# Optimization experiments

Hardware: AMD Instinct MI355X
Metric: run time of the kernel (lower is better)

The kernel has to match this reference:

```python
import jax, jax.numpy as jnp
import numpy as np


def setup_inputs() -> dict:
    key = jax.random.key(0)
    ks = jax.random.split(key, 6)
    N, C, T, V = 32, 64, 128, 25
    F = C * T * V  # 204800
    H = 256
    E = 4
    stdv0 = 1.0 / np.sqrt(F)
    stdv1 = 1.0 / np.sqrt(H)
    stdvA = 1.0 / np.sqrt(V)
    return {
        "x": jax.random.normal(ks[0], (N, C, T, V), dtype=jnp.float32),
        "W0": jax.random.uniform(ks[1], (F, H), jnp.float32, -stdv0, stdv0),
        "b0": jnp.zeros((H,), jnp.float32),
        "W1": jax.random.uniform(ks[2], (H, H), jnp.float32, -stdv1, stdv1),
        "b1": jnp.zeros((H,), jnp.float32),
        "W2": jax.random.uniform(ks[3], (H, E), jnp.float32, -stdv1, stdv1),
        "b2": jnp.zeros((E,), jnp.float32),
        "A": jax.random.uniform(ks[4], (E, T, V, V), jnp.float32, -stdvA, stdvA),
    }


def reference(x, W0, b0, W1, b1, W2, b2, A):
    N = x.shape[0]
    # Gating MLP (dropout treated as identity / eval mode)
    g = x.reshape(N, -1)                      # [N, C*T*V]
    h = jax.nn.elu(g @ W0 + b0)               # [N, 256]
    h = jax.nn.elu(h @ W1 + b1)               # [N, 256]
    logits = h @ W2 + b2                      # [N, 4]
    w = jax.nn.softmax(logits, axis=1)        # [N, 4]
    # Mixture of adjacency experts: AS[n,t,v,w] = sum_e w[n,e] * A[e,t,v,w]
    AS = jnp.einsum('ne,etvw->ntvw', w, A)    # [N, T, V, V]
    # Batched graph convolution
    out = jnp.einsum('nctv,ntvw->nctw', x, AS)
    return out
```

## Files before the change

### kernel.cpp

```cpp
#include <hip/hip_runtime.h>
#include <math.h>

#define Nn 32
#define Cc 64
#define Tt 128
#define Vv 25
#define Kk 204800
#define Hh 256
#define Ee 4
#define KC 256
#define NBLK_A 800

__device__ __forceinline__ float elu1(float v) { return v > 0.0f ? v : expm1f(v); }

__global__ __launch_bounds__(256) void kA(const float* __restrict__ x,
                                          const float* __restrict__ W0,
                                          float* __restrict__ partials) {
  __shared__ float xs[Nn][KC];
  const int tid = threadIdx.x;
  const int b = blockIdx.x;
  const int k0 = b * KC;

  #pragma unroll
  for (int j = tid; j < Nn * (KC / 4); j += 256) {
    int n = j >> 6;
    int c4 = j & 63;
    float4 v = *(const float4*)(x + (size_t)n * Kk + k0 + c4 * 4);
    *(float4*)&xs[n][c4 * 4] = v;
  }
  __syncthreads();

  const int hg = tid & 31;
  const int np = tid >> 5;
  const int h0 = hg * 8;
  const int n0 = np * 4;
  const float* W0p = W0 + (size_t)k0 * Hh + h0;

  float acc[4][8];
  #pragma unroll
  for (int i = 0; i < 4; ++i)
    #pragma unroll
    for (int c = 0; c < 8; ++c) acc[i][c] = 0.0f;

  for (int kk = 0; kk < KC; kk += 4) {
    float4 xv[4];
    #pragma unroll
    for (int i = 0; i < 4; ++i)
      xv[i] = *(const float4*)&xs[n0 + i][kk];
    #pragma unroll
    for (int u = 0; u < 4; ++u) {
      const float* wp = W0p + (size_t)(kk + u) * Hh;
      float4 wa = *(const float4*)(wp);
      float4 wb = *(const float4*)(wp + 4);
      #pragma unroll
      for (int i = 0; i < 4; ++i) {
        float xu = (u == 0) ? xv[i].x : (u == 1) ? xv[i].y : (u == 2) ? xv[i].z : xv[i].w;
        acc[i][0] = fmaf(xu, wa.x, acc[i][0]);
        acc[i][1] = fmaf(xu, wa.y, acc[i][1]);
        acc[i][2] = fmaf(xu, wa.z, acc[i][2]);
        acc[i][3] = fmaf(xu, wa.w, acc[i][3]);
        acc[i][4] = fmaf(xu, wb.x, acc[i][4]);
        acc[i][5] = fmaf(xu, wb.y, acc[i][5]);
        acc[i][6] = fmaf(xu, wb.z, acc[i][6]);
        acc[i][7] = fmaf(xu, wb.w, acc[i][7]);
      }
    }
  }
  #pragma unroll
  for (int i = 0; i < 4; ++i) {
    float* pp = partials + ((size_t)(b * Nn + n0 + i) << 8) + h0;
    *(float4*)(pp)     = make_float4(acc[i][0], acc[i][1], acc[i][2], acc[i][3]);
    *(float4*)(pp + 4) = make_float4(acc[i][4], acc[i][5], acc[i][6], acc[i][7]);
  }
}

__global__ __launch_bounds__(256) void kB1(const float* __restrict__ partials,
                                           const float* __restrict__ b0,
                                           float* __restrict__ hb) {
  const int n  = blockIdx.x >> 3;
  const int hc = blockIdx.x & 7;
  const int tid = threadIdx.x;
  const int hl = tid & 31;
  const int bsub = tid >> 5;
  const int h = hc * 32 + hl;
  float s = 0.0f;
  for (int j = 0; j < 100; ++j) {
    int b = bsub * 100 + j;
    s += partials[((size_t)(b * Nn + n) << 8) + h];
  }
  __shared__ float red[8][32];
  red[bsub][hl] = s;
  __syncthreads();
  if (tid < 32) {
    float tot = 0.0f;
    #pragma unroll
    for (int sI = 0; sI < 8; ++sI) tot += red[sI][tid];
    int hh = hc * 32 + tid;
    hb[n * Hh + hh] = elu1(tot + b0[hh]);
  }
}

__global__ __launch_bounds__(256) void kB2(const float* __restrict__ hb,
                                           const float* __restrict__ W1,
                                           const float* __restrict__ b1,
                                           const float* __restrict__ W2,
                                           const float* __restrict__ b2,
                                           float* __restrict__ wgt) {
  const int n = blockIdx.x;
  const int tid = threadIdx.x;
  __shared__ float hbs[Hh];
  hbs[tid] = hb[n * Hh + tid];
  __syncthreads();
  float s = b1[tid];
  for (int j = 0; j < Hh; ++j) s = fmaf(hbs[j], W1[j * Hh + tid], s);
  float h2 = elu1(s);
  float le[Ee];
  #pragma unroll
  for (int e = 0; e < Ee; ++e) le[e] = h2 * W2[tid * Ee + e];
  __shared__ float red[Ee][4];
  const int lane = tid & 63;
  const int wid  = tid >> 6;
  #pragma unroll
  for (int e = 0; e < Ee; ++e) {
    float v = le[e];
    for (int off = 32; off > 0; off >>= 1) v += __shfl_down(v, off, 64);
    if (lane == 0) red[e][wid] = v;
  }
  __syncthreads();
  if (tid == 0) {
    float lg[Ee];
    float m = -1e30f;
    #pragma unroll
    for (int e = 0; e < Ee; ++e) {
      lg[e] = red[e][0] + red[e][1] + red[e][2] + red[e][3] + b2[e];
      m = fmaxf(m, lg[e]);
    }
    float den = 0.0f;
    #pragma unroll
    for (int e = 0; e < Ee; ++e) { lg[e] = expf(lg[e] - m); den += lg[e]; }
    float inv = 1.0f / den;
    #pragma unroll
    for (int e = 0; e < Ee; ++e) wgt[n * Ee + e] = lg[e] * inv;
  }
}

#define ASW 28
#define XTS 68
__global__ __launch_bounds__(256) void kC(const float* __restrict__ x,
                                          const float* __restrict__ A,
                                          const float* __restrict__ wgt,
                                          float* __restrict__ out) {
  const int blk = blockIdx.x;
  const int n  = blk >> 6;
  const int tp = blk & 63;
  const int tid = threadIdx.x;
  const int tsub = tid >> 7;
  const int tl = tid & 127;
  const int t = tp * 2 + tsub;

  __shared__ float AS[2][Vv][ASW];
  __shared__ float xT[2][Vv][XTS];

  float wv[Ee];
  #pragma unroll
  for (int e = 0; e < Ee; ++e) wv[e] = wgt[n * Ee + e];

  for (int idx = tl; idx < Vv * ASW; idx += 128) {
    int v = idx / ASW;
    int w = idx - v * ASW;
    float s = 0.0f;
    if (w < Vv) {
      #pragma unroll
      for (int e = 0; e < Ee; ++e)
        s = fmaf(wv[e], A[((size_t)(e * Tt + t) * Vv + v) * Vv + w], s);
    }
    AS[tsub][v][w] = s;
  }
  const float* xb = x + (size_t)n * (Cc * Tt * Vv) + (size_t)t * Vv;
  for (int idx = tl; idx < Cc * Vv; idx += 128) {
    int c = idx / Vv;
    int v = idx - c * Vv;
    xT[tsub][v][c] = xb[(size_t)c * (Tt * Vv) + v];
  }
  __syncthreads();

  const int ct = tl & 15;
  const int wq = tl >> 4;
  if (wq < 7) {
    const int c0 = ct * 4;
    const int w0 = wq * 4;
    float acc[4][4];
    #pragma unroll
    for (int i = 0; i < 4; ++i)
      #pragma unroll
      for (int j = 0; j < 4; ++j) acc[i][j] = 0.0f;
    #pragma unroll 5
    for (int v = 0; v < Vv; ++v) {
      float4 a4 = *(const float4*)&AS[tsub][v][w0];
      float4 x4 = *(const float4*)&xT[tsub][v][c0];
      const float xr[4] = {x4.x, x4.y, x4.z, x4.w};
      const float ar[4] = {a4.x, a4.y, a4.z, a4.w};
      #pragma unroll
      for (int i = 0; i < 4; ++i)
        #pragma unroll
        for (int j = 0; j < 4; ++j)
          acc[i][j] = fmaf(xr[i], ar[j], acc[i][j]);
    }
    #pragma unroll
    for (int i = 0; i < 4; ++i) {
      int c = c0 + i;
      float* ob = out + ((size_t)(n * Cc + c) * Tt + t) * Vv;
      #pragma unroll
      for (int j = 0; j < 4; ++j) {
        int w = w0 + j;
        if (w < Vv) ob[w] = acc[i][j];
      }
    }
  }
}

extern "C" void kernel_launch(void* const* d_in, const int* in_sizes, int n_in,
                              void* d_out, int out_size, void* d_ws, size_t ws_size,
                              hipStream_t stream) {
  const float* x  = (const float*)d_in[0];
  const float* W0 = (const float*)d_in[1];
  const float* b0 = (const float*)d_in[2];
  const float* W1 = (const float*)d_in[3];
  const float* b1 = (const float*)d_in[4];
  const float* W2 = (const float*)d_in[5];
  const float* b2 = (const float*)d_in[6];
  const float* A  = (const float*)d_in[7];
  float* out = (float*)d_out;

  float* partials = (float*)d_ws;
  float* hb  = partials + (size_t)NBLK_A * Nn * Hh;
  float* wgt = hb + Nn * Hh;

  kA <<<NBLK_A,  256, 0, stream>>>(x, W0, partials);
  kB1<<<256,     256, 0, stream>>>(partials, b0, hb);
  kB2<<<Nn,      256, 0, stream>>>(hb, W1, b1, W2, b2, wgt);
  kC <<<Nn * 64, 256, 0, stream>>>(x, A, wgt, out);
}
```

Baseline: 426.7 us.

## Double-buffer W0 tiles in LDS via async global_load_lds in kA

Kernel kA now stages the x slice and W0 rows into shared memory with direct global-to-LDS loads. W0 is streamed in 16-row tiles with a two-stage double buffer, so the next tile's load overlaps the FMAs on the current one. Previously every thread read W0 straight from global memory inside the inner loop. The change adds 32KB of LDS and a barrier per step, which may reduce occupancy, and correctness depends on the async LDS writes being visible at the barrier.

```diff
diff --git a/kernel.cpp b/kernel.cpp
--- a/kernel.cpp
+++ b/kernel.cpp
@@ -9,32 +9,39 @@
 #define Hh 256
 #define Ee 4
 #define KC 256
+#define KB 16
+#define NSTEP (KC / KB)
 #define NBLK_A 800
 
 __device__ __forceinline__ float elu1(float v) { return v > 0.0f ? v : expm1f(v); }
+
+typedef const __attribute__((address_space(1))) void* gvp;
+typedef __attribute__((address_space(3))) void* lvp;
+__device__ __forceinline__ void gl_lds16(const void* g, void* l) {
+  __builtin_amdgcn_global_load_lds((gvp)g, (lvp)l, 16, 0, 0);
+}
 
 __global__ __launch_bounds__(256) void kA(const float* __restrict__ x,
                                           const float* __restrict__ W0,
                                           float* __restrict__ partials) {
   __shared__ float xs[Nn][KC];
-  const int tid = threadIdx.x;
-  const int b = blockIdx.x;
+  __shared__ float wbuf[2][KB][Hh];
+  const int tid  = threadIdx.x;
+  const int lane = tid & 63;
+  const int wv   = tid >> 6;
+  const int b  = blockIdx.x;
   const int k0 = b * KC;
 
-  #pragma unroll
-  for (int j = tid; j < Nn * (KC / 4); j += 256) {
-    int n = j >> 6;
-    int c4 = j & 63;
-    float4 v = *(const float4*)(x + (size_t)n * Kk + k0 + c4 * 4);
-    *(float4*)&xs[n][c4 * 4] = v;
-  }
+  for (int r = wv; r < Nn; r += 4)
+    gl_lds16(x + (size_t)r * Kk + k0 + lane * 4, &xs[r][0]);
+  for (int r = wv; r < KB; r += 4)
+    gl_lds16(W0 + (size_t)(k0 + r) * Hh + lane * 4, &wbuf[0][r][0]);
   __syncthreads();
 
   const int hg = tid & 31;
   const int np = tid >> 5;
   const int h0 = hg * 8;
   const int n0 = np * 4;
-  const float* W0p = W0 + (size_t)k0 * Hh + h0;
 
   float acc[4][8];
   #pragma unroll
@@ -42,30 +49,42 @@
     #pragma unroll
     for (int c = 0; c < 8; ++c) acc[i][c] = 0.0f;
 
-  for (int kk = 0; kk < KC; kk += 4) {
-    float4 xv[4];
-    #pragma unroll
-    for (int i = 0; i < 4; ++i)
-      xv[i] = *(const float4*)&xs[n0 + i][kk];
-    #pragma unroll
-    for (int u = 0; u < 4; ++u) {
-      const float* wp = W0p + (size_t)(kk + u) * Hh;
-      float4 wa = *(const float4*)(wp);
-      float4 wb = *(const float4*)(wp + 4);
-      #pragma unroll
-      for (int i = 0; i < 4; ++i) {
-        float xu = (u == 0) ? xv[i].x : (u == 1) ? xv[i].y : (u == 2) ? xv[i].z : xv[i].w;
-        acc[i][0] = fmaf(xu, wa.x, acc[i][0]);
-        acc[i][1] = fmaf(xu, wa.y, acc[i][1]);
-        acc[i][2] = fmaf(xu, wa.z, acc[i][2]);
-        acc[i][3] = fmaf(xu, wa.w, acc[i][3]);
-        acc[i][4] = fmaf(xu, wb.x, acc[i][4]);
-        acc[i][5] = fmaf(xu, wb.y, acc[i][5]);
-        acc[i][6] = fmaf(xu, wb.z, acc[i][6]);
-        acc[i][7] = fmaf(xu, wb.w, acc[i][7]);
+  for (int step = 0; step < NSTEP; ++step) {
+    const int cur = step & 1;
+    if (step + 1 < NSTEP) {
+      const int kb = (step + 1) * KB;
+      for (int r = wv; r < KB; r += 4)
+        gl_lds16(W0 + (size_t)(k0 + kb + r) * Hh + lane * 4, &wbuf[cur ^ 1][r][0]);
+    }
+    const int kbase = step * KB;
+    #pragma unroll
+    for (int kk = 0; kk < KB; kk += 4) {
+      float4 xv[4];
+      #pragma unroll
+      for (int i = 0; i < 4; ++i)
+        xv[i] = *(const float4*)&xs[n0 + i][kbase + kk];
+      #pragma unroll
+      for (int u = 0; u < 4; ++u) {
+        const float* wp = &wbuf[cur][kk + u][h0];
+        float4 wa = *(const float4*)(wp);
+        float4 wb = *(const float4*)(wp + 4);
+        #pragma unroll
+        for (int i = 0; i < 4; ++i) {
+          float xu = (u == 0) ? xv[i].x : (u == 1) ? xv[i].y : (u == 2) ? xv[i].z : xv[i].w;
+          acc[i][0] = fmaf(xu, wa.x, acc[i][0]);
+          acc[i][1] = fmaf(xu, wa.y, acc[i][1]);
+          acc[i][2] = fmaf(xu, wa.z, acc[i][2]);
+          acc[i][3] = fmaf(xu, wa.w, acc[i][3]);
+          acc[i][4] = fmaf(xu, wb.x, acc[i][4]);
+          acc[i][5] = fmaf(xu, wb.y, acc[i][5]);
+          acc[i][6] = fmaf(xu, wb.z, acc[i][6]);
+          acc[i][7] = fmaf(xu, wb.w, acc[i][7]);
+        }
       }
     }
-  }
+    __syncthreads();
+  }
+
   #pragma unroll
   for (int i = 0; i < 4; ++i) {
     float* pp = partials + ((size_t)(b * Nn + n0 + i) << 8) + h0;
```

Result: faster. 379.1 us (-11.1%).

## Halve K-chunk, load x tile directly to LDS, retile kA thread mapping

Applied to the files above, without the earlier changes.

Halves the K chunk per block in the first GEMV kernel, doubling the block count to 1600 for more parallelism. The x tile is staged with the global_load_lds builtin so data goes straight from global memory into shared memory without passing through registers. The thread mapping changes so each lane owns 4 contiguous hidden columns and each wave owns 8 batch rows, which makes W0 loads fully coalesced 16-byte loads across a wave. The cost is twice as many partial sums, which doubles the partials traffic written by kA and read back by the reduction kernel.

```diff
diff --git a/kernel.cpp b/kernel.cpp
--- a/kernel.cpp
+++ b/kernel.cpp
@@ -8,70 +8,72 @@
 #define Kk 204800
 #define Hh 256
 #define Ee 4
-#define KC 256
-#define NBLK_A 800
+#define KC 128
+#define NBLK_A 1600
 
 __device__ __forceinline__ float elu1(float v) { return v > 0.0f ? v : expm1f(v); }
+
+typedef const __attribute__((address_space(1))) void* gvp;
+typedef __attribute__((address_space(3))) void* lvp;
+__device__ __forceinline__ void gl_lds16(const void* g, void* l) {
+  __builtin_amdgcn_global_load_lds((gvp)g, (lvp)l, 16, 0, 0);
+}
+
+typedef float v4f __attribute__((ext_vector_type(4)));
 
 __global__ __launch_bounds__(256) void kA(const float* __restrict__ x,
                                           const float* __restrict__ W0,
                                           float* __restrict__ partials) {
   __shared__ float xs[Nn][KC];
-  const int tid = threadIdx.x;
-  const int b = blockIdx.x;
+  const int tid  = threadIdx.x;
+  const int lane = tid & 63;
+  const int wv   = tid >> 6;
+  const int b  = blockIdx.x;
   const int k0 = b * KC;
 
-  #pragma unroll
-  for (int j = tid; j < Nn * (KC / 4); j += 256) {
-    int n = j >> 6;
-    int c4 = j & 63;
-    float4 v = *(const float4*)(x + (size_t)n * Kk + k0 + c4 * 4);
-    *(float4*)&xs[n][c4 * 4] = v;
-  }
-  __syncthreads();
-
-  const int hg = tid & 31;
-  const int np = tid >> 5;
-  const int h0 = hg * 8;
-  const int n0 = np * 4;
+  for (int rp = wv; rp < 16; rp += 4) {
+    const int row = 2 * rp + (lane >> 5);
+    gl_lds16(x + (size_t)row * Kk + k0 + (lane & 31) * 4, &xs[2 * rp][0]);
+  }
+
+  const int h0 = lane * 4;
+  const int n0 = wv * 8;
   const float* W0p = W0 + (size_t)k0 * Hh + h0;
 
-  float acc[4][8];
-  #pragma unroll
-  for (int i = 0; i < 4; ++i)
-    #pragma unroll
-    for (int c = 0; c < 8; ++c) acc[i][c] = 0.0f;
-
+  float acc[8][4];
+  #pragma unroll
+  for (int i = 0; i < 8; ++i)
+    #pragma unroll
+    for (int c = 0; c < 4; ++c) acc[i][c] = 0.0f;
+
+  __syncthreads();
+
+  #pragma unroll 2
   for (int kk = 0; kk < KC; kk += 4) {
-    float4 xv[4];
-    #pragma unroll
-    for (int i = 0; i < 4; ++i)
-      xv[i] = *(const float4*)&xs[n0 + i][kk];
-    #pragma unroll
-    for (int u = 0; u < 4; ++u) {
-      const float* wp = W0p + (size_t)(kk + u) * Hh;
-      float4 wa = *(const float4*)(wp);
-      float4 wb = *(const float4*)(wp + 4);
-      #pragma unroll
-      for (int i = 0; i < 4; ++i) {
-        float xu = (u == 0) ? xv[i].x : (u == 1) ? xv[i].y : (u == 2) ? xv[i].z : xv[i].w;
-        acc[i][0] = fmaf(xu, wa.x, acc[i][0]);
-        acc[i][1] = fmaf(xu, wa.y, acc[i][1]);
-        acc[i][2] = fmaf(xu, wa.z, acc[i][2]);
-        acc[i][3] = fmaf(xu, wa.w, acc[i][3]);
-        acc[i][4] = fmaf(xu, wb.x, acc[i][4]);
-        acc[i][5] = fmaf(xu, wb.y, acc[i][5]);
-        acc[i][6] = fmaf(xu, wb.z, acc[i][6]);
-        acc[i][7] = fmaf(xu, wb.w, acc[i][7]);
+    v4f wr[4];
+    #pragma unroll
+    for (int u = 0; u < 4; ++u)
+      wr[u] = *(const v4f*)(W0p + (size_t)(kk + u) * Hh);
+    v4f xv[8];
+    #pragma unroll
+    for (int i = 0; i < 8; ++i)
+      xv[i] = *(const v4f*)&xs[n0 + i][kk];
+    #pragma unroll
+    for (int u = 0; u < 4; ++u)
+      #pragma unroll
+      for (int i = 0; i < 8; ++i) {
+        float xu = xv[i][u];
+        acc[i][0] = fmaf(xu, wr[u][0], acc[i][0]);
+        acc[i][1] = fmaf(xu, wr[u][1], acc[i][1]);
+        acc[i][2] = fmaf(xu, wr[u][2], acc[i][2]);
+        acc[i][3] = fmaf(xu, wr[u][3], acc[i][3]);
       }
-    }
-  }
-  #pragma unroll
-  for (int i = 0; i < 4; ++i) {
-    float* pp = partials + ((size_t)(b * Nn + n0 + i) << 8) + h0;
-    *(float4*)(pp)     = make_float4(acc[i][0], acc[i][1], acc[i][2], acc[i][3]);
-    *(float4*)(pp + 4) = make_float4(acc[i][4], acc[i][5], acc[i][6], acc[i][7]);
-  }
+  }
+
+  #pragma unroll
+  for (int i = 0; i < 8; ++i)
+    *(v4f*)&partials[((size_t)(b * Nn + n0 + i) << 8) + h0] =
+        (v4f){acc[i][0], acc[i][1], acc[i][2], acc[i][3]};
 }
 
 __global__ __launch_bounds__(256) void kB1(const float* __restrict__ partials,
@@ -84,8 +86,8 @@
   const int bsub = tid >> 5;
   const int h = hc * 32 + hl;
   float s = 0.0f;
-  for (int j = 0; j < 100; ++j) {
-    int b = bsub * 100 + j;
+  for (int j = 0; j < 200; ++j) {
+    int b = bsub * 200 + j;
     s += partials[((size_t)(b * Nn + n) << 8) + h];
   }
   __shared__ float red[8][32];
```

Measured after the change: 409.0 us. 4.2% less time.
